# Kernel optimization log

Measured on AMD Instinct MI355X. Metric: run time of the kernel, lower is better.

Reference implementation:

```python
import jax, jax.numpy as jnp
import numpy as np

N = 50000
E = 800000
IN_C = 64
HID = 64
HEADS = 4
NUM_GRAPHS = 64
NEG_SLOPE = 0.2


def setup_inputs() -> dict:
    key = jax.random.key(0)
    ks = jax.random.split(key, 16)
    x = jax.random.normal(ks[0], (N, IN_C), dtype=jnp.float32)
    edge_index = jax.random.randint(ks[1], (2, E), 0, N, dtype=jnp.int64)
    batch = jnp.sort(jax.random.randint(ks[2], (N,), 0, NUM_GRAPHS, dtype=jnp.int64))
    s = lambda *sh: 1.0 / np.sqrt(sh[0])
    # conv1: in -> HID per head, concat -> HEADS*HID
    W1 = jax.random.normal(ks[3], (IN_C, HEADS * HID), dtype=jnp.float32) * s(IN_C)
    a1_src = jax.random.normal(ks[4], (HEADS, HID), dtype=jnp.float32) * s(HID)
    a1_dst = jax.random.normal(ks[5], (HEADS, HID), dtype=jnp.float32) * s(HID)
    b1 = jnp.zeros((HEADS * HID,), dtype=jnp.float32)
    # conv2: HEADS*HID -> HID, single head, no concat
    W2 = jax.random.normal(ks[6], (HEADS * HID, HID), dtype=jnp.float32) * s(HEADS * HID)
    a2_src = jax.random.normal(ks[7], (1, HID), dtype=jnp.float32) * s(HID)
    a2_dst = jax.random.normal(ks[8], (1, HID), dtype=jnp.float32) * s(HID)
    b2 = jnp.zeros((HID,), dtype=jnp.float32)
    # MLP head: HID -> 16 -> 1
    Wh1 = jax.random.normal(ks[9], (HID, 16), dtype=jnp.float32) * s(HID)
    bh1 = jnp.zeros((16,), dtype=jnp.float32)
    Wh2 = jax.random.normal(ks[10], (16, 1), dtype=jnp.float32) * s(16)
    bh2 = jnp.zeros((1,), dtype=jnp.float32)
    return {"x": x, "edge_index": edge_index, "batch": batch,
            "W1": W1, "a1_src": a1_src, "a1_dst": a1_dst, "b1": b1,
            "W2": W2, "a2_src": a2_src, "a2_dst": a2_dst, "b2": b2,
            "Wh1": Wh1, "bh1": bh1, "Wh2": Wh2, "bh2": bh2}


def _gat_conv(x, src, dst, W, a_src, a_dst, b, concat):
    """PyG-style GATConv (eval mode, self-loops already appended)."""
    H, C = a_src.shape
    xp = (x @ W).reshape(-1, H, C)                      # [N,H,C]
    e_s = jnp.einsum('nhc,hc->nh', xp, a_src)            # source contribution
    e_d = jnp.einsum('nhc,hc->nh', xp, a_dst)            # target contribution
    e = jax.nn.leaky_relu(e_s[src] + e_d[dst], NEG_SLOPE)  # [E,H]
    # segment softmax over edges grouped by destination node
    m = jax.ops.segment_max(e, dst, num_segments=N)
    ex = jnp.exp(e - m[dst])
    denom = jax.ops.segment_sum(ex, dst, num_segments=N)
    alpha = ex / denom[dst]                              # [E,H]
    out = jax.ops.segment_sum(alpha[:, :, None] * xp[src], dst, num_segments=N)  # [N,H,C]
    out = out.reshape(-1, H * C) if concat else out.mean(axis=1)
    return out + b


def reference(x, edge_index, batch, W1, a1_src, a1_dst, b1,
              W2, a2_src, a2_dst, b2, Wh1, bh1, Wh2, bh2):
    # add self loops once (GATConv default add_self_loops=True)
    loop = jnp.arange(N, dtype=edge_index.dtype)
    src = jnp.concatenate([edge_index[0], loop])
    dst = jnp.concatenate([edge_index[1], loop])
    h = jax.nn.elu(_gat_conv(x, src, dst, W1, a1_src, a1_dst, b1, concat=True))
    h = _gat_conv(h, src, dst, W2, a2_src, a2_dst, b2, concat=False)
    # global mean pool over graphs
    summed = jax.ops.segment_sum(h, batch, num_segments=NUM_GRAPHS)
    cnt = jax.ops.segment_sum(jnp.ones((N,), h.dtype), batch, num_segments=NUM_GRAPHS)
    pooled = summed / jnp.maximum(cnt, 1.0)[:, None]     # [G,HID]
    z = jax.nn.relu(pooled @ Wh1 + bh1)
    out = jax.nn.sigmoid(z @ Wh2 + bh2)
    return out.squeeze(-1)                               # [G]
```

## Files before the change

### kernel.cpp

```cpp
#include <hip/hip_runtime.h>
#include <math.h>

#define N_NODES 50000
#define N_EDGES 800000
#define EA (N_EDGES + N_NODES)
#define HEADS 4
#define HID 64
#define NG 64
#define NEG_SLOPE 0.2f
#define SCAN_CHUNK 1024
#define NBLK ((N_NODES + SCAN_CHUNK - 1) / SCAN_CHUNK)

typedef _Float16 f16x8 __attribute__((ext_vector_type(8)));
typedef float f32x4 __attribute__((ext_vector_type(4)));
struct h4 { _Float16 a, b, c, d; };

__device__ inline float lrelu(float x) { return x > 0.f ? x : NEG_SLOPE * x; }

__device__ inline void edge_sd(const int* __restrict__ ei, int e, int& s, int& d) {
    if (e < N_EDGES) { s = ei[e]; d = ei[N_EDGES + e]; }
    else { s = e - N_EDGES; d = s; }
}

__device__ inline f16x8 ldfrag(const _Float16* __restrict__ p, int lq) {
    uint2 lo = *(const uint2*)(p + lq * 4);
    uint2 hi = *(const uint2*)(p + 16 + lq * 4);
    union { uint4 u; f16x8 v; } f;
    f.u = make_uint4(lo.x, lo.y, hi.x, hi.y);
    return f.v;
}

__global__ void k_zero(int* __restrict__ deg, float* __restrict__ pooled,
                       float* __restrict__ cnt)
{
    int i = blockIdx.x * 256 + threadIdx.x;
    int st = gridDim.x * 256;
    for (int j = i; j < N_NODES; j += st) deg[j] = 0;
    if (i < NG * HID) pooled[i] = 0.f;
    if (i < NG) cnt[i] = 0.f;
}

__global__ void k_deg(const int* __restrict__ ei, int* __restrict__ deg)
{
    int e = blockIdx.x * 256 + threadIdx.x;
    if (e >= EA) return;
    int s, d; edge_sd(ei, e, s, d);
    atomicAdd(&deg[d], 1);
}

__global__ __launch_bounds__(1024) void k_scan1(const int* __restrict__ deg,
        int* __restrict__ incl, int* __restrict__ blksum)
{
    __shared__ int sd[SCAN_CHUNK];
    int t = threadIdx.x;
    int i = blockIdx.x * SCAN_CHUNK + t;
    sd[t] = (i < N_NODES) ? deg[i] : 0;
    for (int off = 1; off < SCAN_CHUNK; off <<= 1) {
        __syncthreads();
        int u = (t >= off) ? sd[t - off] : 0;
        __syncthreads();
        sd[t] += u;
    }
    if (i < N_NODES) incl[i] = sd[t];
    if (t == SCAN_CHUNK - 1) blksum[blockIdx.x] = sd[t];
}

__global__ void k_scan2(const int* __restrict__ blksum, int* __restrict__ blkoff)
{
    if (threadIdx.x == 0) {
        int acc = 0;
        for (int b = 0; b < NBLK; ++b) { blkoff[b] = acc; acc += blksum[b]; }
    }
}

__global__ void k_scan3(const int* __restrict__ incl, const int* __restrict__ blkoff,
                        const int* __restrict__ deg, const int* __restrict__ batch,
                        int* __restrict__ rowptr, int* __restrict__ cursor,
                        float* __restrict__ cnt)
{
    int i = blockIdx.x * 256 + threadIdx.x;
    bool act = i < N_NODES;
    if (act) {
        int v = incl[i] + blkoff[i >> 10];
        rowptr[i + 1] = v;
        cursor[i] = v - deg[i];
        if (i == 0) rowptr[0] = 0;
    }
    int g = act ? batch[i] : -1;
    int lane = threadIdx.x & 63;
    int g0 = __shfl(g, 0, 64);
    if (__all(g == g0)) {
        if (lane == 0 && g0 >= 0) atomicAdd(&cnt[g0], 64.f);
    } else if (act) {
        atomicAdd(&cnt[g], 1.f);
    }
}

__global__ void k_fill(const int* __restrict__ ei, int* __restrict__ cursor,
                       int* __restrict__ csr_src)
{
    int e = blockIdx.x * 256 + threadIdx.x;
    if (e >= EA) return;
    int s, d; edge_sd(ei, e, s, d);
    int pos = atomicAdd(&cursor[d], 1);
    csr_src[pos] = s;
}

__global__ __launch_bounds__(256) void k_prepw(const float* __restrict__ W1,
        const float* __restrict__ a1s, const float* __restrict__ a1d,
        const float* __restrict__ W2, const float* __restrict__ a2s,
        const float* __restrict__ a2d, _Float16* __restrict__ W1P,
        _Float16* __restrict__ W2P, float* __restrict__ va1s,
        float* __restrict__ va1d, float* __restrict__ va2s, float* __restrict__ va2d)
{
    const int t = threadIdx.x;
    for (int i = t; i < 256 * 64; i += 256) {
        int np = i >> 6, k = i & 63;
        W1P[i] = (_Float16)W1[k * 256 + (np & 3) * 64 + (np >> 2)];
    }
    for (int i = t; i < 64 * 256; i += 256) {
        int n = i >> 8, k = i & 255;
        W2P[i] = (_Float16)W2[k * 64 + n];
    }
    {
        int k = t >> 2, h = t & 3;
        float ss = 0.f, sd = 0.f;
        for (int c = 0; c < 64; ++c) {
            float wv = W1[k * 256 + h * 64 + c];
            ss = fmaf(wv, a1s[h * 64 + c], ss);
            sd = fmaf(wv, a1d[h * 64 + c], sd);
        }
        va1s[k * 4 + h] = ss;
        va1d[k * 4 + h] = sd;
    }
    {
        float ss = 0.f, sd = 0.f;
        for (int c = 0; c < 64; ++c) {
            float wv = W2[t * 64 + c];
            ss = fmaf(wv, a2s[c], ss);
            sd = fmaf(wv, a2d[c], sd);
        }
        va2s[t] = ss;
        va2d[t] = sd;
    }
}

__global__ __launch_bounds__(256) void k_prepx(const float* __restrict__ x,
        const float* __restrict__ va1s, const float* __restrict__ va1d,
        _Float16* __restrict__ xh, float* __restrict__ e1s, float* __restrict__ e1d)
{
    const int lane = threadIdx.x & 63;
    const int w = threadIdx.x >> 6;
    const int n = blockIdx.x * 4 + w;
    if (n >= N_NODES) return;
    float xv = x[(size_t)n * 64 + lane];
    xh[(size_t)n * 64 + lane] = (_Float16)xv;
    float4 vs = ((const float4*)va1s)[lane];
    float4 vd = ((const float4*)va1d)[lane];
    float s0 = xv * vs.x, s1 = xv * vs.y, s2 = xv * vs.z, s3 = xv * vs.w;
    float d0 = xv * vd.x, d1 = xv * vd.y, d2 = xv * vd.z, d3 = xv * vd.w;
    #pragma unroll
    for (int off = 32; off > 0; off >>= 1) {
        s0 += __shfl_down(s0, off, 64); s1 += __shfl_down(s1, off, 64);
        s2 += __shfl_down(s2, off, 64); s3 += __shfl_down(s3, off, 64);
        d0 += __shfl_down(d0, off, 64); d1 += __shfl_down(d1, off, 64);
        d2 += __shfl_down(d2, off, 64); d3 += __shfl_down(d3, off, 64);
    }
    if (lane == 0) {
        ((float4*)e1s)[n] = make_float4(s0, s1, s2, s3);
        ((float4*)e1d)[n] = make_float4(d0, d1, d2, d3);
    }
}

__global__ __launch_bounds__(256) void k_gemm1(const _Float16* __restrict__ xh,
        const _Float16* __restrict__ W1P, _Float16* __restrict__ xp1h)
{
    const int t = threadIdx.x;
    const int lane = t & 63, w = t >> 6;
    const int l15 = lane & 15, lq = lane >> 4;
    const int m0 = blockIdx.x * 64 + w * 16;
    const int mrow = m0 + l15;
    const _Float16* xrow = xh + (size_t)(m0 + l15) * 64;
    f16x8 xf0 = ldfrag(xrow, lq);
    f16x8 xf1 = ldfrag(xrow + 32, lq);
    #pragma unroll
    for (int ct = 0; ct < 16; ++ct) {
        const _Float16* wrow = W1P + (size_t)(ct * 16 + l15) * 64;
        f16x8 wf0 = ldfrag(wrow, lq);
        f16x8 wf1 = ldfrag(wrow + 32, lq);
        f32x4 acc = {0.f, 0.f, 0.f, 0.f};
        acc = __builtin_amdgcn_mfma_f32_16x16x32_f16(wf0, xf0, acc, 0, 0, 0);
        acc = __builtin_amdgcn_mfma_f32_16x16x32_f16(wf1, xf1, acc, 0, 0, 0);
        if (mrow < N_NODES) {
            h4 o = {(_Float16)acc[0], (_Float16)acc[1], (_Float16)acc[2], (_Float16)acc[3]};
            *(h4*)(xp1h + (size_t)mrow * 256 + ct * 16 + lq * 4) = o;
        }
    }
}

__global__ void k_att1(const int* __restrict__ rowptr, const int* __restrict__ csr_src,
                       const float* __restrict__ e1s, const float* __restrict__ e1d,
                       float* __restrict__ alpha1, float* __restrict__ rinv1)
{
    int d = blockIdx.x * 256 + threadIdx.x;
    if (d >= N_NODES) return;
    int beg = rowptr[d], end = rowptr[d + 1];
    float4 ed = ((const float4*)e1d)[d];
    float4 sum = make_float4(0.f, 0.f, 0.f, 0.f);
    for (int j = beg; j < end; ++j) {
        int s = csr_src[j];
        float4 q = ((const float4*)e1s)[s];
        float4 p;
        p.x = __expf(lrelu(q.x + ed.x));
        p.y = __expf(lrelu(q.y + ed.y));
        p.z = __expf(lrelu(q.z + ed.z));
        p.w = __expf(lrelu(q.w + ed.w));
        sum.x += p.x; sum.y += p.y; sum.z += p.z; sum.w += p.w;
        ((float4*)alpha1)[j] = p;
    }
    ((float4*)rinv1)[d] = make_float4(1.f / sum.x, 1.f / sum.y, 1.f / sum.z, 1.f / sum.w);
}

__global__ __launch_bounds__(256) void k_aggr1(const int* __restrict__ rowptr,
        const int* __restrict__ csr_src, const float* __restrict__ alpha1,
        const float* __restrict__ rinv1, const _Float16* __restrict__ xp1h,
        const float* __restrict__ b1, const float* __restrict__ va2s,
        const float* __restrict__ va2d, _Float16* __restrict__ h1h,
        float* __restrict__ e2s, float* __restrict__ e2d)
{
    const int lane = threadIdx.x & 63;
    const int w = __builtin_amdgcn_readfirstlane(threadIdx.x >> 6);
    const int d = blockIdx.x * 4 + w;
    if (d >= N_NODES) return;
    const int beg = rowptr[d], end = rowptr[d + 1];
    float a0 = 0.f, a1 = 0.f, a2 = 0.f, a3 = 0.f;
    #pragma unroll 2
    for (int j = beg; j < end; ++j) {
        int s = csr_src[j];
        float4 al = ((const float4*)alpha1)[j];
        h4 xv = *(const h4*)(xp1h + (size_t)s * 256 + lane * 4);
        a0 = fmaf(al.x, (float)xv.a, a0);
        a1 = fmaf(al.y, (float)xv.b, a1);
        a2 = fmaf(al.z, (float)xv.c, a2);
        a3 = fmaf(al.w, (float)xv.d, a3);
    }
    float4 iv = ((const float4*)rinv1)[d];
    float acc[4] = {a0 * iv.x, a1 * iv.y, a2 * iv.z, a3 * iv.w};
    float es = 0.f, edd = 0.f;
    #pragma unroll
    for (int hh = 0; hh < 4; ++hh) {
        float v = acc[hh] + b1[hh * 64 + lane];
        v = v > 0.f ? v : __expf(v) - 1.f;
        h1h[(size_t)d * 256 + hh * 64 + lane] = (_Float16)v;
        es  = fmaf(v, va2s[hh * 64 + lane], es);
        edd = fmaf(v, va2d[hh * 64 + lane], edd);
    }
    #pragma unroll
    for (int off = 32; off > 0; off >>= 1) {
        es += __shfl_down(es, off, 64);
        edd += __shfl_down(edd, off, 64);
    }
    if (lane == 0) { e2s[d] = es; e2d[d] = edd; }
}

__global__ __launch_bounds__(256) void k_gemm2(const _Float16* __restrict__ h1h,
        const _Float16* __restrict__ W2P, _Float16* __restrict__ xp2h)
{
    const int t = threadIdx.x;
    const int lane = t & 63, w = t >> 6;
    const int l15 = lane & 15, lq = lane >> 4;
    const int m0 = blockIdx.x * 64 + w * 16;
    const int mrow = m0 + l15;
    const _Float16* arow = h1h + (size_t)(m0 + l15) * 256;
    f16x8 af[8];
    #pragma unroll
    for (int ks = 0; ks < 8; ++ks) af[ks] = ldfrag(arow + ks * 32, lq);
    #pragma unroll
    for (int ct = 0; ct < 4; ++ct) {
        const _Float16* wrow = W2P + (size_t)(ct * 16 + l15) * 256;
        f32x4 acc = {0.f, 0.f, 0.f, 0.f};
        #pragma unroll
        for (int ks = 0; ks < 8; ++ks) {
            f16x8 wf = ldfrag(wrow + ks * 32, lq);
            acc = __builtin_amdgcn_mfma_f32_16x16x32_f16(wf, af[ks], acc, 0, 0, 0);
        }
        if (mrow < N_NODES) {
            h4 o = {(_Float16)acc[0], (_Float16)acc[1], (_Float16)acc[2], (_Float16)acc[3]};
            *(h4*)(xp2h + (size_t)mrow * 64 + ct * 16 + lq * 4) = o;
        }
    }
}

__global__ void k_att2(const int* __restrict__ rowptr, const int* __restrict__ csr_src,
                       const float* __restrict__ e2s, const float* __restrict__ e2d,
                       float* __restrict__ alpha2, float* __restrict__ rinv2)
{
    int d = blockIdx.x * 256 + threadIdx.x;
    if (d >= N_NODES) return;
    int beg = rowptr[d], end = rowptr[d + 1];
    float ed = e2d[d];
    float sum = 0.f;
    for (int j = beg; j < end; ++j) {
        float p = __expf(lrelu(e2s[csr_src[j]] + ed));
        sum += p;
        alpha2[j] = p;
    }
    rinv2[d] = 1.f / sum;
}

__global__ __launch_bounds__(256) void k_aggr2(const int* __restrict__ rowptr,
        const int* __restrict__ csr_src, const float* __restrict__ alpha2,
        const float* __restrict__ rinv2, const _Float16* __restrict__ xp2h,
        const float* __restrict__ b2, const int* __restrict__ batch,
        float* __restrict__ pooled)
{
    const int lane = threadIdx.x & 63;
    const int w = __builtin_amdgcn_readfirstlane(threadIdx.x >> 6);
    const int d = blockIdx.x * 4 + w;
    if (d >= N_NODES) return;
    const int beg = rowptr[d], end = rowptr[d + 1];
    float acc = 0.f;
    #pragma unroll 2
    for (int j = beg; j < end; ++j) {
        int s = csr_src[j];
        float al = alpha2[j];
        acc = fmaf(al, (float)xp2h[(size_t)s * 64 + lane], acc);
    }
    float val = acc * rinv2[d] + b2[lane];
    int g = batch[d];
    atomicAdd(&pooled[g * 64 + lane], val);
}

__global__ void k_mlp(const float* __restrict__ pooled, const float* __restrict__ cnt,
                      const float* __restrict__ Wh1, const float* __restrict__ bh1,
                      const float* __restrict__ Wh2, const float* __restrict__ bh2,
                      float* __restrict__ out)
{
    int g = threadIdx.x;
    float inv = 1.f / fmaxf(cnt[g], 1.f);
    float p[64];
    #pragma unroll
    for (int c = 0; c < 64; ++c) p[c] = pooled[g * 64 + c] * inv;
    float acc2 = bh2[0];
    for (int j = 0; j < 16; ++j) {
        float z = bh1[j];
        #pragma unroll
        for (int c = 0; c < 64; ++c) z = fmaf(p[c], Wh1[c * 16 + j], z);
        z = fmaxf(z, 0.f);
        acc2 = fmaf(z, Wh2[j], acc2);
    }
    out[g] = 1.f / (1.f + expf(-acc2));
}

extern "C" void kernel_launch(void* const* d_in, const int* in_sizes, int n_in,
                              void* d_out, int out_size, void* d_ws, size_t ws_size,
                              hipStream_t stream)
{
    const float* x      = (const float*)d_in[0];
    const int*   ei     = (const int*)d_in[1];
    const int*   batch  = (const int*)d_in[2];
    const float* W1     = (const float*)d_in[3];
    const float* a1s    = (const float*)d_in[4];
    const float* a1d    = (const float*)d_in[5];
    const float* b1     = (const float*)d_in[6];
    const float* W2     = (const float*)d_in[7];
    const float* a2s    = (const float*)d_in[8];
    const float* a2d    = (const float*)d_in[9];
    const float* b2     = (const float*)d_in[10];
    const float* Wh1    = (const float*)d_in[11];
    const float* bh1    = (const float*)d_in[12];
    const float* Wh2    = (const float*)d_in[13];
    const float* bh2    = (const float*)d_in[14];
    float* out = (float*)d_out;

    float* ws = (float*)d_ws;
    size_t off = 0;
    _Float16* xp1h = (_Float16*)(ws + off); off += (size_t)N_NODES * 128;
    _Float16* h1h  = (_Float16*)(ws + off); off += (size_t)(N_NODES + 64) * 128;
    _Float16* xh   = (_Float16*)(ws + off); off += (size_t)(N_NODES + 64) * 32;
    float* e1s    = ws + off; off += (size_t)N_NODES * 4;
    float* e1d    = ws + off; off += (size_t)N_NODES * 4;
    float* rinv1  = ws + off; off += (size_t)N_NODES * 4;
    float* alpha1 = ws + off; off += (size_t)EA * 4;
    float* e2s    = ws + off; off += N_NODES;
    float* e2d    = ws + off; off += N_NODES;
    float* rinv2  = ws + off; off += N_NODES;
    float* alpha2 = ws + off; off += EA;
    _Float16* xp2h = (_Float16*)(ws + off); off += (size_t)N_NODES * 32;
    _Float16* W1P  = (_Float16*)(ws + off); off += 8192;
    _Float16* W2P  = (_Float16*)(ws + off); off += 8192;
    float* va1s   = ws + off; off += 256;
    float* va1d   = ws + off; off += 256;
    float* va2s   = ws + off; off += 256;
    float* va2d   = ws + off; off += 256;
    float* pooled = ws + off; off += NG * HID;
    float* cnt    = ws + off; off += NG;
    int* rowptr   = (int*)(ws + off); off += N_NODES + 2;
    int* cursor   = (int*)(ws + off); off += N_NODES;
    int* csr_src  = (int*)(ws + off); off += EA;
    int* blksum   = (int*)(ws + off); off += NBLK;
    int* blkoff   = (int*)(ws + off); off += NBLK;
    int* deg  = (int*)alpha1;
    int* incl = deg + N_NODES;

    const int BE = (EA + 255) / 256;
    const int BN = (N_NODES + 255) / 256;
    const int BW = (N_NODES + 3) / 4;
    const int BG = (N_NODES + 63) / 64;

    hipLaunchKernelGGL(k_zero,  dim3(64),   dim3(256),  0, stream, deg, pooled, cnt);
    hipLaunchKernelGGL(k_deg,   dim3(BE),   dim3(256),  0, stream, ei, deg);
    hipLaunchKernelGGL(k_scan1, dim3(NBLK), dim3(1024), 0, stream, deg, incl, blksum);
    hipLaunchKernelGGL(k_scan2, dim3(1),    dim3(64),   0, stream, blksum, blkoff);
    hipLaunchKernelGGL(k_scan3, dim3(BN),   dim3(256),  0, stream,
                       incl, blkoff, deg, batch, rowptr, cursor, cnt);
    hipLaunchKernelGGL(k_fill,  dim3(BE),   dim3(256),  0, stream, ei, cursor, csr_src);

    hipLaunchKernelGGL(k_prepw, dim3(1),  dim3(256), 0, stream,
                       W1, a1s, a1d, W2, a2s, a2d, W1P, W2P, va1s, va1d, va2s, va2d);
    hipLaunchKernelGGL(k_prepx, dim3(BW), dim3(256), 0, stream,
                       x, va1s, va1d, xh, e1s, e1d);
    hipLaunchKernelGGL(k_gemm1, dim3(BG), dim3(256), 0, stream, xh, W1P, xp1h);
    hipLaunchKernelGGL(k_att1,  dim3(BN), dim3(256), 0, stream,
                       rowptr, csr_src, e1s, e1d, alpha1, rinv1);
    hipLaunchKernelGGL(k_aggr1, dim3(BW), dim3(256), 0, stream,
                       rowptr, csr_src, alpha1, rinv1, xp1h, b1, va2s, va2d,
                       h1h, e2s, e2d);
    hipLaunchKernelGGL(k_gemm2, dim3(BG), dim3(256), 0, stream, h1h, W2P, xp2h);
    hipLaunchKernelGGL(k_att2,  dim3(BN), dim3(256), 0, stream,
                       rowptr, csr_src, e2s, e2d, alpha2, rinv2);
    hipLaunchKernelGGL(k_aggr2, dim3(BW), dim3(256), 0, stream,
                       rowptr, csr_src, alpha2, rinv2, xp2h, b2, batch, pooled);

    hipLaunchKernelGGL(k_mlp, dim3(1), dim3(64), 0, stream,
                       pooled, cnt, Wh1, bh1, Wh2, bh2, out);
}
```

Baseline: 511.9 us.

## Fuse attention softmax computation into aggregation kernels via wave-cooperative shuffles

Removes the separate k_att1/k_att2 kernels and their alpha/rinv buffers. Each aggregation wave now loads up to 64 edge sources and attention logits cooperatively, one per lane, computes the exponentials in parallel, then broadcasts them with shuffles while accumulating both the weighted features and the softmax denominator. This drops two launches and the write and re-read of the per-edge alpha arrays, at the cost of extra shuffle instructions and padded iterations. The deg scratch is moved onto h1h since alpha1 no longer exists.

New measurement: 444.8 us. -13.1%, faster.

```diff
diff --git a/kernel.cpp b/kernel.cpp
--- a/kernel.cpp
+++ b/kernel.cpp
@@ -198,54 +198,53 @@
     }
 }
 
-__global__ void k_att1(const int* __restrict__ rowptr, const int* __restrict__ csr_src,
-                       const float* __restrict__ e1s, const float* __restrict__ e1d,
-                       float* __restrict__ alpha1, float* __restrict__ rinv1)
-{
-    int d = blockIdx.x * 256 + threadIdx.x;
-    if (d >= N_NODES) return;
-    int beg = rowptr[d], end = rowptr[d + 1];
-    float4 ed = ((const float4*)e1d)[d];
-    float4 sum = make_float4(0.f, 0.f, 0.f, 0.f);
-    for (int j = beg; j < end; ++j) {
-        int s = csr_src[j];
-        float4 q = ((const float4*)e1s)[s];
-        float4 p;
-        p.x = __expf(lrelu(q.x + ed.x));
-        p.y = __expf(lrelu(q.y + ed.y));
-        p.z = __expf(lrelu(q.z + ed.z));
-        p.w = __expf(lrelu(q.w + ed.w));
-        sum.x += p.x; sum.y += p.y; sum.z += p.z; sum.w += p.w;
-        ((float4*)alpha1)[j] = p;
-    }
-    ((float4*)rinv1)[d] = make_float4(1.f / sum.x, 1.f / sum.y, 1.f / sum.z, 1.f / sum.w);
-}
-
 __global__ __launch_bounds__(256) void k_aggr1(const int* __restrict__ rowptr,
-        const int* __restrict__ csr_src, const float* __restrict__ alpha1,
-        const float* __restrict__ rinv1, const _Float16* __restrict__ xp1h,
+        const int* __restrict__ csr_src, const float* __restrict__ e1s,
+        const float* __restrict__ e1d, const _Float16* __restrict__ xp1h,
         const float* __restrict__ b1, const float* __restrict__ va2s,
         const float* __restrict__ va2d, _Float16* __restrict__ h1h,
-        float* __restrict__ e2s, float* __restrict__ e2d)
+        float* __restrict__ e2s_o, float* __restrict__ e2d_o)
 {
     const int lane = threadIdx.x & 63;
     const int w = __builtin_amdgcn_readfirstlane(threadIdx.x >> 6);
     const int d = blockIdx.x * 4 + w;
     if (d >= N_NODES) return;
     const int beg = rowptr[d], end = rowptr[d + 1];
+    const float4 ed = ((const float4*)e1d)[d];
     float a0 = 0.f, a1 = 0.f, a2 = 0.f, a3 = 0.f;
-    #pragma unroll 2
-    for (int j = beg; j < end; ++j) {
-        int s = csr_src[j];
-        float4 al = ((const float4*)alpha1)[j];
-        h4 xv = *(const h4*)(xp1h + (size_t)s * 256 + lane * 4);
-        a0 = fmaf(al.x, (float)xv.a, a0);
-        a1 = fmaf(al.y, (float)xv.b, a1);
-        a2 = fmaf(al.z, (float)xv.c, a2);
-        a3 = fmaf(al.w, (float)xv.d, a3);
-    }
-    float4 iv = ((const float4*)rinv1)[d];
-    float acc[4] = {a0 * iv.x, a1 * iv.y, a2 * iv.z, a3 * iv.w};
+    float d0 = 0.f, d1 = 0.f, d2 = 0.f, d3 = 0.f;
+    for (int jb = beg; jb < end; jb += 64) {
+        int myj = jb + lane;
+        int sv = 0;
+        float4 p = make_float4(0.f, 0.f, 0.f, 0.f);
+        if (myj < end) {
+            sv = csr_src[myj];
+            float4 q = ((const float4*)e1s)[sv];
+            p.x = __expf(lrelu(q.x + ed.x));
+            p.y = __expf(lrelu(q.y + ed.y));
+            p.z = __expf(lrelu(q.z + ed.z));
+            p.w = __expf(lrelu(q.w + ed.w));
+        }
+        int nj = end - jb; if (nj > 64) nj = 64;
+        int njr = (nj + 3) & ~3;
+        for (int j = 0; j < njr; j += 4) {
+            #pragma unroll
+            for (int k = 0; k < 4; ++k) {
+                int s = __shfl(sv, j + k, 64);
+                float px = __shfl(p.x, j + k, 64);
+                float py = __shfl(p.y, j + k, 64);
+                float pz = __shfl(p.z, j + k, 64);
+                float pw = __shfl(p.w, j + k, 64);
+                h4 xv = *(const h4*)(xp1h + (size_t)s * 256 + lane * 4);
+                a0 = fmaf(px, (float)xv.a, a0);
+                a1 = fmaf(py, (float)xv.b, a1);
+                a2 = fmaf(pz, (float)xv.c, a2);
+                a3 = fmaf(pw, (float)xv.d, a3);
+                d0 += px; d1 += py; d2 += pz; d3 += pw;
+            }
+        }
+    }
+    float acc[4] = {a0 / d0, a1 / d1, a2 / d2, a3 / d3};
     float es = 0.f, edd = 0.f;
     #pragma unroll
     for (int hh = 0; hh < 4; ++hh) {
@@ -260,7 +259,7 @@
         es += __shfl_down(es, off, 64);
         edd += __shfl_down(edd, off, 64);
     }
-    if (lane == 0) { e2s[d] = es; e2d[d] = edd; }
+    if (lane == 0) { e2s_o[d] = es; e2d_o[d] = edd; }
 }
 
 __global__ __launch_bounds__(256) void k_gemm2(const _Float16* __restrict__ h1h,
@@ -291,26 +290,9 @@
     }
 }
 
-__global__ void k_att2(const int* __restrict__ rowptr, const int* __restrict__ csr_src,
-                       const float* __restrict__ e2s, const float* __restrict__ e2d,
-                       float* __restrict__ alpha2, float* __restrict__ rinv2)
-{
-    int d = blockIdx.x * 256 + threadIdx.x;
-    if (d >= N_NODES) return;
-    int beg = rowptr[d], end = rowptr[d + 1];
-    float ed = e2d[d];
-    float sum = 0.f;
-    for (int j = beg; j < end; ++j) {
-        float p = __expf(lrelu(e2s[csr_src[j]] + ed));
-        sum += p;
-        alpha2[j] = p;
-    }
-    rinv2[d] = 1.f / sum;
-}
-
 __global__ __launch_bounds__(256) void k_aggr2(const int* __restrict__ rowptr,
-        const int* __restrict__ csr_src, const float* __restrict__ alpha2,
-        const float* __restrict__ rinv2, const _Float16* __restrict__ xp2h,
+        const int* __restrict__ csr_src, const float* __restrict__ e2s,
+        const float* __restrict__ e2d, const _Float16* __restrict__ xp2h,
         const float* __restrict__ b2, const int* __restrict__ batch,
         float* __restrict__ pooled)
 {
@@ -319,14 +301,29 @@
     const int d = blockIdx.x * 4 + w;
     if (d >= N_NODES) return;
     const int beg = rowptr[d], end = rowptr[d + 1];
-    float acc = 0.f;
-    #pragma unroll 2
-    for (int j = beg; j < end; ++j) {
-        int s = csr_src[j];
-        float al = alpha2[j];
-        acc = fmaf(al, (float)xp2h[(size_t)s * 64 + lane], acc);
-    }
-    float val = acc * rinv2[d] + b2[lane];
+    const float ed = e2d[d];
+    float acc = 0.f, den = 0.f;
+    for (int jb = beg; jb < end; jb += 64) {
+        int myj = jb + lane;
+        int sv = 0;
+        float p = 0.f;
+        if (myj < end) {
+            sv = csr_src[myj];
+            p = __expf(lrelu(e2s[sv] + ed));
+        }
+        int nj = end - jb; if (nj > 64) nj = 64;
+        int njr = (nj + 7) & ~7;
+        for (int j = 0; j < njr; j += 8) {
+            #pragma unroll
+            for (int k = 0; k < 8; ++k) {
+                int s = __shfl(sv, j + k, 64);
+                float pv = __shfl(p, j + k, 64);
+                acc = fmaf(pv, (float)xp2h[(size_t)s * 64 + lane], acc);
+                den += pv;
+            }
+        }
+    }
+    float val = acc / den + b2[lane];
     int g = batch[d];
     atomicAdd(&pooled[g * 64 + lane], val);
 }
@@ -380,12 +377,8 @@
     _Float16* xh   = (_Float16*)(ws + off); off += (size_t)(N_NODES + 64) * 32;
     float* e1s    = ws + off; off += (size_t)N_NODES * 4;
     float* e1d    = ws + off; off += (size_t)N_NODES * 4;
-    float* rinv1  = ws + off; off += (size_t)N_NODES * 4;
-    float* alpha1 = ws + off; off += (size_t)EA * 4;
     float* e2s    = ws + off; off += N_NODES;
     float* e2d    = ws + off; off += N_NODES;
-    float* rinv2  = ws + off; off += N_NODES;
-    float* alpha2 = ws + off; off += EA;
     _Float16* xp2h = (_Float16*)(ws + off); off += (size_t)N_NODES * 32;
     _Float16* W1P  = (_Float16*)(ws + off); off += 8192;
     _Float16* W2P  = (_Float16*)(ws + off); off += 8192;
@@ -400,7 +393,7 @@
     int* csr_src  = (int*)(ws + off); off += EA;
     int* blksum   = (int*)(ws + off); off += NBLK;
     int* blkoff   = (int*)(ws + off); off += NBLK;
-    int* deg  = (int*)alpha1;
+    int* deg  = (int*)h1h;
     int* incl = deg + N_NODES;
 
     const int BE = (EA + 255) / 256;
@@ -421,16 +414,12 @@
     hipLaunchKernelGGL(k_prepx, dim3(BW), dim3(256), 0, stream,
                        x, va1s, va1d, xh, e1s, e1d);
     hipLaunchKernelGGL(k_gemm1, dim3(BG), dim3(256), 0, stream, xh, W1P, xp1h);
-    hipLaunchKernelGGL(k_att1,  dim3(BN), dim3(256), 0, stream,
-                       rowptr, csr_src, e1s, e1d, alpha1, rinv1);
     hipLaunchKernelGGL(k_aggr1, dim3(BW), dim3(256), 0, stream,
-                       rowptr, csr_src, alpha1, rinv1, xp1h, b1, va2s, va2d,
+                       rowptr, csr_src, e1s, e1d, xp1h, b1, va2s, va2d,
                        h1h, e2s, e2d);
     hipLaunchKernelGGL(k_gemm2, dim3(BG), dim3(256), 0, stream, h1h, W2P, xp2h);
-    hipLaunchKernelGGL(k_att2,  dim3(BN), dim3(256), 0, stream,
-                       rowptr, csr_src, e2s, e2d, alpha2, rinv2);
     hipLaunchKernelGGL(k_aggr2, dim3(BW), dim3(256), 0, stream,
-                       rowptr, csr_src, alpha2, rinv2, xp2h, b2, batch, pooled);
+                       rowptr, csr_src, e2s, e2d, xp2h, b2, batch, pooled);
 
     hipLaunchKernelGGL(k_mlp, dim3(1), dim3(64), 0, stream,
                        pooled, cnt, Wh1, bh1, Wh2, bh2, out);
```
